# Kernel tuning notes

Hardware: AMD Instinct MI355X
Metric: run time of the kernel (lower is better)

## Reference

```python
import jax, jax.numpy as jnp
import numpy as np

N, FIN, H, C, D = 50000, 128, 4, 64, 4
E = 800000


def leaky_relu(x, slope):
    return jnp.where(x >= 0, x, slope * x)


def gat_layer(x, src, dst, W, A, att_src, att_dst, bias):
    # x: [N, Fin]; W: [Fin, H*C]; A: [Fin, H*D]; att_*: [H, D]; bias: [C]
    n = x.shape[0]
    h = (x @ W).reshape(n, H, -1)          # [N, H, C] message features
    a = (x @ A).reshape(n, H, -1)          # [N, H, D] attention features
    alpha_src = jnp.einsum('nhd,hd->nh', a, att_src)   # [N, H]
    alpha_dst = jnp.einsum('nhd,hd->nh', a, att_dst)   # [N, H]
    e = leaky_relu(alpha_src[src] + alpha_dst[dst], 0.2)  # [E, H]
    # edge softmax over incoming edges of each destination node
    m = jax.ops.segment_max(e, dst, num_segments=n)       # [N, H]
    ex = jnp.exp(e - m[dst])                               # [E, H]
    denom = jax.ops.segment_sum(ex, dst, num_segments=n)  # [N, H]
    w = ex / denom[dst]                                    # [E, H]
    msg = h[src] * w[..., None]                            # [E, H, C]
    out = jax.ops.segment_sum(msg, dst, num_segments=n)   # [N, H, C]
    return out.mean(axis=1) + bias                         # head-average -> [N, C]


def setup_inputs() -> dict:
    key = jax.random.key(0)
    ks = jax.random.split(key, 12)
    x = jax.random.normal(ks[0], (N, FIN), dtype=jnp.float32)
    edge_index = jax.random.randint(ks[1], (2, E), 0, N, dtype=jnp.int64)
    s = 0.05
    return {
        'x': x,
        'edge_index': edge_index,
        'W1': jax.random.normal(ks[2], (FIN, H * C), dtype=jnp.float32) * s,
        'A1': jax.random.normal(ks[3], (FIN, H * D), dtype=jnp.float32) * s,
        'att_src1': jax.random.normal(ks[4], (H, D), dtype=jnp.float32) * s,
        'att_dst1': jax.random.normal(ks[5], (H, D), dtype=jnp.float32) * s,
        'b1': jnp.zeros((C,), dtype=jnp.float32),
        'W2': jax.random.normal(ks[6], (C, H * C), dtype=jnp.float32) * s,
        'A2': jax.random.normal(ks[7], (C, H * D), dtype=jnp.float32) * s,
        'att_src2': jax.random.normal(ks[8], (H, D), dtype=jnp.float32) * s,
        'att_dst2': jax.random.normal(ks[9], (H, D), dtype=jnp.float32) * s,
        'b2': jnp.zeros((C,), dtype=jnp.float32),
    }


def reference(x, edge_index, W1, A1, att_src1, att_dst1, b1, W2, A2, att_src2, att_dst2, b2):
    src, dst = edge_index[0], edge_index[1]
    x = gat_layer(x, src, dst, W1, A1, att_src1, att_dst1, b1)
    x = leaky_relu(x, 0.1)
    x = gat_layer(x, src, dst, W2, A2, att_src2, att_dst2, b2)
    x = leaky_relu(x, 0.1)
    return x
```

## Files before the change

kernel.cpp:

```cpp
#include <hip/hip_runtime.h>


#define N_NODES 50000
#define N_EDGES 800000
#define CAP 64
#define NB_SC4 782
#define NB_NODE1 782

typedef __attribute__((ext_vector_type(8))) short short8;
typedef __attribute__((ext_vector_type(8))) _Float16 f16x8;
typedef __attribute__((ext_vector_type(2))) _Float16 f16x2;
typedef __attribute__((ext_vector_type(4))) float f32x4;
typedef __attribute__((ext_vector_type(8))) unsigned short ushort8;
typedef __attribute__((ext_vector_type(4))) unsigned short us4v;

__device__ __forceinline__ float bf2f(unsigned short u){
  return __uint_as_float(((unsigned int)u) << 16);
}
__device__ __forceinline__ unsigned short f2bf(float f){
  unsigned int u = __float_as_uint(f);
  u = (u + 0x7FFFu + ((u >> 16) & 1u)) >> 16;
  return (unsigned short)u;
}
__device__ __forceinline__ float ldf(const void* p, int i, bool bf){
  return bf ? bf2f(((const unsigned short*)p)[i]) : ((const float*)p)[i];
}
__device__ __forceinline__ float rdlane(float v, int lane){
  return __uint_as_float(__builtin_amdgcn_readlane(__float_as_uint(v), lane));
}

struct SetupPtrs {
  const void *W1, *A1, *aS1, *aD1, *b1, *W2, *A2, *aS2, *aD2, *b2, *x;
};

__global__ __launch_bounds__(256) void k_setup(SetupPtrs S,
    _Float16* __restrict__ Wb1f, _Float16* __restrict__ Wb2f,
    unsigned short* __restrict__ Bsd1f, unsigned short* __restrict__ Bsd2f,
    float* __restrict__ bc1, float* __restrict__ bc2,
    int* __restrict__ flag)
{
  __shared__ int sbf;
  const int tid = threadIdx.x;
  if (tid < 64){
    unsigned int w = ((const unsigned int*)S.x)[tid] & 0xFFFFu;
    unsigned int e = (w >> 7) & 0xFFu;
    bool hit = (e >= 100u && e <= 135u);
    unsigned long long m = __ballot(hit);
    if (tid == 0) sbf = (__popcll(m) > 40) ? 1 : 0;
  }
  __syncthreads();
  const bool bf = (sbf != 0);
  const int bw = blockIdx.x;
  if (bw < 128){
    int t = bw * 256 + tid;
    int j = t & 7, lane = (t >> 3) & 63, kt = (t >> 9) & 15, nt = t >> 13;
    int q = kt * 32 + (lane >> 4) * 8 + j;
    int c = nt * 16 + (lane & 15);
    int h = q >> 7, f = q & 127;
    Wb1f[t] = (_Float16)(0.25f * ldf(S.W1, f * 256 + h * 64 + c, bf));
  } else if (bw < 192){
    int t = (bw - 128) * 256 + tid;
    int j = t & 7, lane = (t >> 3) & 63, kt = (t >> 9) & 7, nt = t >> 12;
    int q = kt * 32 + (lane >> 4) * 8 + j;
    int c = nt * 16 + (lane & 15);
    int h = q >> 6, f = q & 63;
    Wb2f[t] = (_Float16)(0.25f * ldf(S.W2, f * 256 + h * 64 + c, bf));
  } else if (bw < 200){
    int t = (bw - 192) * 256 + tid;
    int j = t & 7, lane = (t >> 3) & 63, kt = t >> 9;
    int k = kt * 32 + (lane >> 4) * 8 + j;
    int c = lane & 15;
    float v = 0.f;
    if (c < 4){
      for (int dd = 0; dd < 4; ++dd)
        v += ldf(S.A1, k * 16 + c * 4 + dd, bf) * ldf(S.aS1, c * 4 + dd, bf);
    } else if (c < 8){
      int h = c - 4;
      for (int dd = 0; dd < 4; ++dd)
        v += ldf(S.A1, k * 16 + h * 4 + dd, bf) * ldf(S.aD1, h * 4 + dd, bf);
    }
    Bsd1f[t] = f2bf(v);
  } else if (bw < 204){
    int t = (bw - 200) * 256 + tid;
    int j = t & 7, lane = (t >> 3) & 63, kt = t >> 9;
    int k = kt * 32 + (lane >> 4) * 8 + j;
    int c = lane & 15;
    float v = 0.f;
    if (c < 4){
      for (int dd = 0; dd < 4; ++dd)
        v += ldf(S.A2, k * 16 + c * 4 + dd, bf) * ldf(S.aS2, c * 4 + dd, bf);
    } else if (c < 8){
      int h = c - 4;
      for (int dd = 0; dd < 4; ++dd)
        v += ldf(S.A2, k * 16 + h * 4 + dd, bf) * ldf(S.aD2, h * 4 + dd, bf);
    }
    Bsd2f[t] = f2bf(v);
  } else {
    if (tid < 64)       bc1[tid] = ldf(S.b1, tid, bf);
    else if (tid < 128) bc2[tid - 64] = ldf(S.b2, tid - 64, bf);
    else if (tid == 128) *flag = bf ? 1 : 0;
  }
}


template<int F, bool DYN>
__device__ __forceinline__ void nodeA_body(int nblk, int tid,
    const void* __restrict__ xin_, const unsigned short* __restrict__ Bsdf,
    float* __restrict__ alpha_s, float* __restrict__ alpha_d,
    const int* __restrict__ flag)
{
  const int STR = F + 8;
  const int KT  = F / 32;
  const int CH  = F / 8;
  __shared__ unsigned short xs[64 * (F + 8)];
  const int base = nblk * 64;
  bool bf = true;
  if (DYN) bf = (*flag != 0);
  for (int v = tid; v < 64 * CH; v += 256){
    int row = v / CH, c8 = v % CH;
    int node = base + row; if (node >= N_NODES) node = N_NODES - 1;
    size_t g = (size_t)node * F + c8 * 8;
    ushort8 u;
    if (!DYN || bf){
      u = *(const ushort8*)((const unsigned short*)xin_ + g);
    } else {
      const float* xf = (const float*)xin_ + g;
      float4 f0 = *(const float4*)xf, f1 = *(const float4*)(xf + 4);
      u[0]=f2bf(f0.x); u[1]=f2bf(f0.y); u[2]=f2bf(f0.z); u[3]=f2bf(f0.w);
      u[4]=f2bf(f1.x); u[5]=f2bf(f1.y); u[6]=f2bf(f1.z); u[7]=f2bf(f1.w);
    }
    *(ushort8*)&xs[row * STR + c8 * 8] = u;
  }
  __syncthreads();

  const int wave = tid >> 6, l = tid & 63;
  const int quad = l >> 4, m = l & 15;
  const int wbase = base + wave * 16;

  f32x4 aacc = (f32x4)0.f;
  #pragma unroll
  for (int kt = 0; kt < KT; ++kt){
    short8 af = *(const short8*)&xs[(wave * 16 + m) * STR + kt * 32 + quad * 8];
    short8 sdfrag = *(const short8*)(Bsdf + ((size_t)kt * 64 + l) * 8);
    aacc = __builtin_amdgcn_mfma_f32_16x16x32_bf16(af, sdfrag, aacc, 0, 0, 0);
  }
  if (m < 8){
    float* dstp = (m < 4) ? alpha_s : alpha_d;
    int hh = m & 3;
    #pragma unroll
    for (int r = 0; r < 4; ++r){
      int node = wbase + quad * 4 + r;
      if (node < N_NODES) dstp[node * 4 + hh] = aacc[r];
    }
  }
}


__global__ __launch_bounds__(256) void k_scatter_nodeA1(
    const int* __restrict__ src, const int* __restrict__ dst,
    int* __restrict__ fill, unsigned short* __restrict__ csr,
    const void* __restrict__ xin_, const unsigned short* __restrict__ Bsdf,
    float* __restrict__ alpha_s, float* __restrict__ alpha_d,
    const int* __restrict__ flag)
{
  const int b = blockIdx.x, tid = threadIdx.x;
  if (b < NB_SC4){
    const int ebase = b * 1024 + tid;
    int d[4], s[4];
    #pragma unroll
    for (int i = 0; i < 4; ++i){
      int e = ebase + i * 256;
      bool ok = (e < N_EDGES);
      d[i] = ok ? dst[e] : -1;
      s[i] = ok ? src[e] : 0;
    }
    #pragma unroll
    for (int i = 0; i < 4; ++i){
      if (d[i] >= 0){
        int r = atomicAdd(&fill[d[i]], 1);
        if (r < CAP) csr[((unsigned)d[i] << 6) + r] = (unsigned short)s[i];
      }
    }
    return;
  }
  nodeA_body<128, true>(b - NB_SC4, tid, xin_, Bsdf, alpha_s, alpha_d, flag);
}

template<int F, bool DYN>
__global__ __launch_bounds__(256) void k_nodeA(const void* __restrict__ xin_,
    const unsigned short* __restrict__ Bsdf,
    float* __restrict__ alpha_s, float* __restrict__ alpha_d,
    const int* __restrict__ flag)
{
  nodeA_body<F, DYN>(blockIdx.x, threadIdx.x, xin_, Bsdf, alpha_s, alpha_d, flag);
}


template<int FIN, bool BF>
__device__ __forceinline__ void ldrow(const void* xg, unsigned s, int f0,
                                      float (&out)[FIN / 16])
{
  const int NFL = FIN / 16;
  if (BF){
    const unsigned short* p = (const unsigned short*)xg + (size_t)s * FIN + f0;
    if (NFL == 8){
      ushort8 u = *(const ushort8*)p;
      #pragma unroll
      for (int j = 0; j < NFL; ++j) out[j] = bf2f(u[j]);
    } else {
      us4v u = *(const us4v*)p;
      #pragma unroll
      for (int j = 0; j < NFL; ++j) out[j] = bf2f(u[j]);
    }
  } else {
    const float* p = (const float*)xg + (size_t)s * FIN + f0;
    #pragma unroll
    for (int j = 0; j < NFL; ++j) out[j] = p[j];
  }
}

template<bool BF, int STR>
__device__ __forceinline__ void aggr_phase1_u128(const void* __restrict__ xg,
    const float* __restrict__ alpha_s, const float* __restrict__ alpha_d,
    const int* __restrict__ fill, const unsigned short* __restrict__ csr,
    _Float16* __restrict__ ylds, int base, int w, int l)
{
  const int h = l >> 4;
  #pragma unroll 1
  for (int r = 0; r < 4; ++r){
    const int n = base + w * 4 + r;
    const float adv = alpha_d[n * 4 + h];
    float den = 0.f;
    float acc[4][2];
    #pragma unroll
    for (int hh = 0; hh < 4; ++hh){ acc[hh][0] = 0.f; acc[hh][1] = 0.f; }

    int cnt = fill[n]; if (cnt > CAP) cnt = CAP;
    const unsigned short* cp = csr + ((unsigned)n << 6);
    int p = 0;
    for (; p + 8 <= cnt; p += 8){
      ushort8 s8 = *(const ushort8*)(cp + p);
      float a[8];
      float lo[8], hi[8];
      #pragma unroll
      for (int i = 0; i < 8; ++i){
        unsigned s = s8[i];
        a[i] = alpha_s[s * 4 + h];
        if (BF){
          unsigned xv = *(const unsigned int*)((const unsigned short*)xg + (size_t)s * 128 + 2 * l);
          lo[i] = bf2f((unsigned short)(xv & 0xFFFFu));
          hi[i] = bf2f((unsigned short)(xv >> 16));
        } else {
          const float* xf = (const float*)xg + (size_t)s * 128 + 2 * l;
          lo[i] = xf[0]; hi[i] = xf[1];
        }
      }
      #pragma unroll
      for (int i = 0; i < 8; ++i){
        float e = a[i] + adv; e = fmaxf(e, 0.2f * e); float wt = __expf(e);
        den += wt;
        float w0 = rdlane(wt, 0),  w1 = rdlane(wt, 16);
        float w2 = rdlane(wt, 32), w3 = rdlane(wt, 48);
        acc[0][0] += w0 * lo[i]; acc[0][1] += w0 * hi[i];
        acc[1][0] += w1 * lo[i]; acc[1][1] += w1 * hi[i];
        acc[2][0] += w2 * lo[i]; acc[2][1] += w2 * hi[i];
        acc[3][0] += w3 * lo[i]; acc[3][1] += w3 * hi[i];
      }
    }
    if (p + 4 <= cnt){
      ushort4 s4 = *(const ushort4*)(cp + p);
      unsigned ss[4] = {s4.x, s4.y, s4.z, s4.w};
      float a[4], lo[4], hi[4];
      #pragma unroll
      for (int i = 0; i < 4; ++i){
        a[i] = alpha_s[ss[i] * 4 + h];
        if (BF){
          unsigned xv = *(const unsigned int*)((const unsigned short*)xg + (size_t)ss[i] * 128 + 2 * l);
          lo[i] = bf2f((unsigned short)(xv & 0xFFFFu));
          hi[i] = bf2f((unsigned short)(xv >> 16));
        } else {
          const float* xf = (const float*)xg + (size_t)ss[i] * 128 + 2 * l;
          lo[i] = xf[0]; hi[i] = xf[1];
        }
      }
      #pragma unroll
      for (int i = 0; i < 4; ++i){
        float e = a[i] + adv; e = fmaxf(e, 0.2f * e); float wt = __expf(e);
        den += wt;
        float w0 = rdlane(wt, 0),  w1 = rdlane(wt, 16);
        float w2 = rdlane(wt, 32), w3 = rdlane(wt, 48);
        acc[0][0] += w0 * lo[i]; acc[0][1] += w0 * hi[i];
        acc[1][0] += w1 * lo[i]; acc[1][1] += w1 * hi[i];
        acc[2][0] += w2 * lo[i]; acc[2][1] += w2 * hi[i];
        acc[3][0] += w3 * lo[i]; acc[3][1] += w3 * hi[i];
      }
      p += 4;
    }
    for (; p < cnt; ++p){
      unsigned s = cp[p];
      float a = alpha_s[s * 4 + h];
      float lo, hi;
      if (BF){
        unsigned xv = *(const unsigned int*)((const unsigned short*)xg + (size_t)s * 128 + 2 * l);
        lo = bf2f((unsigned short)(xv & 0xFFFFu));
        hi = bf2f((unsigned short)(xv >> 16));
      } else {
        const float* xf = (const float*)xg + (size_t)s * 128 + 2 * l;
        lo = xf[0]; hi = xf[1];
      }
      float e = a + adv; e = fmaxf(e, 0.2f * e); float wt = __expf(e);
      den += wt;
      float w0 = rdlane(wt, 0),  w1 = rdlane(wt, 16);
      float w2 = rdlane(wt, 32), w3 = rdlane(wt, 48);
      acc[0][0] += w0 * lo; acc[0][1] += w0 * hi;
      acc[1][0] += w1 * lo; acc[1][1] += w1 * hi;
      acc[2][0] += w2 * lo; acc[2][1] += w2 * hi;
      acc[3][0] += w3 * lo; acc[3][1] += w3 * hi;
    }
    float d0 = rdlane(den, 0),  d1 = rdlane(den, 16);
    float d2 = rdlane(den, 32), d3 = rdlane(den, 48);
    float rh0 = (d0 > 0.f) ? (1.f / d0) : 0.f;
    float rh1 = (d1 > 0.f) ? (1.f / d1) : 0.f;
    float rh2 = (d2 > 0.f) ? (1.f / d2) : 0.f;
    float rh3 = (d3 > 0.f) ? (1.f / d3) : 0.f;
    const int row = w * 4 + r;
    _Float16* yp = &ylds[row * STR + 2 * l];
    *(f16x2*)(yp +   0) = (f16x2){(_Float16)(acc[0][0] * rh0), (_Float16)(acc[0][1] * rh0)};
    *(f16x2*)(yp + 128) = (f16x2){(_Float16)(acc[1][0] * rh1), (_Float16)(acc[1][1] * rh1)};
    *(f16x2*)(yp + 256) = (f16x2){(_Float16)(acc[2][0] * rh2), (_Float16)(acc[2][1] * rh2)};
    *(f16x2*)(yp + 384) = (f16x2){(_Float16)(acc[3][0] * rh3), (_Float16)(acc[3][1] * rh3)};
  }
}

template<int FIN, bool BF, int STR>
__device__ __forceinline__ void aggr_phase1(const void* __restrict__ xg,
    const float* __restrict__ alpha_s, const float* __restrict__ alpha_d,
    const int* __restrict__ fill, const unsigned short* __restrict__ csr,
    _Float16* __restrict__ ylds, int base, int w, int l)
{
  const int NFL = FIN / 16;
  const int h = l >> 4, sub = l & 15, f0 = sub * NFL;
  #pragma unroll 1
  for (int r = 0; r < 4; ++r){
    const int n = base + w * 4 + r;
    const float adv = alpha_d[n * 4 + h];
    float den = 0.f;
    float acc[NFL];
    #pragma unroll
    for (int j = 0; j < NFL; ++j) acc[j] = 0.f;

    int cnt = fill[n]; if (cnt > CAP) cnt = CAP;
    const unsigned short* cp = csr + ((unsigned)n << 6);
    int p = 0;
    for (; p + 8 <= cnt; p += 8){
      ushort8 s8 = *(const ushort8*)(cp + p);
      float a[8];
      float v[8][NFL];
      #pragma unroll
      for (int i = 0; i < 8; ++i){
        unsigned s = s8[i];
        a[i] = alpha_s[s * 4 + h];
        ldrow<FIN, BF>(xg, s, f0, v[i]);
      }
      #pragma unroll
      for (int i = 0; i < 8; ++i){
        float e = a[i] + adv; e = fmaxf(e, 0.2f * e); float wt = __expf(e);
        den += wt;
        #pragma unroll
        for (int j = 0; j < NFL; ++j) acc[j] += wt * v[i][j];
      }
    }
    if (p + 4 <= cnt){
      ushort4 s4 = *(const ushort4*)(cp + p);
      unsigned sx = s4.x, sy = s4.y, sz = s4.z, sw = s4.w;
      float ax = alpha_s[sx * 4 + h];
      float ay = alpha_s[sy * 4 + h];
      float az = alpha_s[sz * 4 + h];
      float aw = alpha_s[sw * 4 + h];
      float vx[NFL], vy[NFL], vz[NFL], vw[NFL];
      ldrow<FIN, BF>(xg, sx, f0, vx);
      ldrow<FIN, BF>(xg, sy, f0, vy);
      ldrow<FIN, BF>(xg, sz, f0, vz);
      ldrow<FIN, BF>(xg, sw, f0, vw);
      float e0 = ax + adv; e0 = fmaxf(e0, 0.2f * e0); float w0 = __expf(e0);
      float e1 = ay + adv; e1 = fmaxf(e1, 0.2f * e1); float w1 = __expf(e1);
      float e2 = az + adv; e2 = fmaxf(e2, 0.2f * e2); float w2 = __expf(e2);
      float e3 = aw + adv; e3 = fmaxf(e3, 0.2f * e3); float w3 = __expf(e3);
      den += w0; den += w1; den += w2; den += w3;
      #pragma unroll
      for (int j = 0; j < NFL; ++j)
        acc[j] += w0 * vx[j] + w1 * vy[j] + w2 * vz[j] + w3 * vw[j];
      p += 4;
    }
    for (; p < cnt; ++p){
      unsigned s = cp[p];
      float a = alpha_s[s * 4 + h];
      float v0[NFL];
      ldrow<FIN, BF>(xg, s, f0, v0);
      float e = a + adv; e = fmaxf(e, 0.2f * e); float wgt = __expf(e);
      den += wgt;
      #pragma unroll
      for (int j = 0; j < NFL; ++j) acc[j] += wgt * v0[j];
    }
    const float rh = (den > 0.f) ? (1.f / den) : 0.f;
    const int row = w * 4 + r;
    _Float16* yp = &ylds[row * STR + h * FIN + f0];
    #pragma unroll
    for (int j = 0; j < NFL; ++j) yp[j] = (_Float16)(acc[j] * rh);
  }
}

template<int FIN, int MODE>
__global__ __launch_bounds__(256) void k_aggrX(
    const void* __restrict__ xg,
    const float* __restrict__ alpha_s, const float* __restrict__ alpha_d,
    const int* __restrict__ fill, const unsigned short* __restrict__ csr,
    const _Float16* __restrict__ Wf,
    const float* __restrict__ bias, void* __restrict__ out,
    const int* __restrict__ flag)
{
  const int K = 4 * FIN, KT = K / 32, STR = K + 8;
  __shared__ _Float16 ylds[16 * (4 * FIN + 8)];
  const int tid = threadIdx.x, w = tid >> 6, l = tid & 63;
  const int base = blockIdx.x * 16;

  if (FIN == 128){
    if (MODE == 0 && *flag == 0)
      aggr_phase1_u128<false, STR>(xg, alpha_s, alpha_d, fill, csr, ylds, base, w, l);
    else
      aggr_phase1_u128<true,  STR>(xg, alpha_s, alpha_d, fill, csr, ylds, base, w, l);
  } else {
    if (MODE == 0 && *flag == 0)
      aggr_phase1<FIN, false, STR>(xg, alpha_s, alpha_d, fill, csr, ylds, base, w, l);
    else
      aggr_phase1<FIN, true,  STR>(xg, alpha_s, alpha_d, fill, csr, ylds, base, w, l);
  }
  __syncthreads();

  const int quad = l >> 4, m = l & 15;
  const int nt = w;
  f32x4 cacc = (f32x4)0.f;
  #pragma unroll
  for (int kt = 0; kt < KT; ++kt){
    f16x8 av = *(const f16x8*)&ylds[m * STR + kt * 32 + quad * 8];
    f16x8 bv = *(const f16x8*)(Wf + ((size_t)(nt * KT + kt) * 64 + l) * 8);
    cacc = __builtin_amdgcn_mfma_f32_16x16x32_f16(av, bv, cacc, 0, 0, 0);
  }
  const int c = nt * 16 + m;
  const float bs = bias[c];
  #pragma unroll
  for (int r2 = 0; r2 < 4; ++r2){
    int node = base + quad * 4 + r2;
    float v = cacc[r2] + bs;
    v = fmaxf(v, 0.1f * v);
    if (MODE == 0){
      ((unsigned short*)out)[(size_t)node * 64 + c] = f2bf(v);
    } else {
      if (*flag) ((unsigned short*)out)[(size_t)node * 64 + c] = f2bf(v);
      else       ((float*)out)[(size_t)node * 64 + c] = v;
    }
  }
}


extern "C" void kernel_launch(void* const* d_in, const int* in_sizes, int n_in,
                              void* d_out, int out_size, void* d_ws, size_t ws_size,
                              hipStream_t stream)
{
  const void* x  = d_in[0];
  const int* ei  = (const int*)d_in[1];
  const int* src = ei;
  const int* dst = ei + N_EDGES;

  char* ws = (char*)d_ws;
  unsigned short* csr = (unsigned short*)(ws);
  unsigned short* x2  = (unsigned short*)(ws + 6400000);
  float* as_    = (float*)(ws + 12800000);
  float* ad_    = (float*)(ws + 13600000);
  int*   fill   = (int*)  (ws + 14400000);
  _Float16* Wb1f = (_Float16*)(ws + 14600000);
  _Float16* Wb2f = (_Float16*)(ws + 14665536);
  unsigned short* Bsd1f = (unsigned short*)(ws + 14698304);
  unsigned short* Bsd2f = (unsigned short*)(ws + 14702400);
  float* bc1    = (float*)(ws + 14704448);
  float* bc2    = (float*)(ws + 14704704);
  int*   flag   = (int*)  (ws + 14704960);

  hipMemsetAsync(fill, 0, N_NODES * sizeof(int), stream);

  SetupPtrs S;
  S.W1 = d_in[2];  S.A1 = d_in[3];  S.aS1 = d_in[4];  S.aD1 = d_in[5];  S.b1 = d_in[6];
  S.W2 = d_in[7];  S.A2 = d_in[8];  S.aS2 = d_in[9];  S.aD2 = d_in[10]; S.b2 = d_in[11];
  S.x  = x;
  k_setup<<<205, 256, 0, stream>>>(S, Wb1f, Wb2f, Bsd1f, Bsd2f, bc1, bc2, flag);

  k_scatter_nodeA1<<<NB_SC4 + NB_NODE1, 256, 0, stream>>>(
      src, dst, fill, csr, x, Bsd1f, as_, ad_, flag);

  k_aggrX<128, 0><<<N_NODES / 16, 256, 0, stream>>>(
      x, as_, ad_, fill, csr, Wb1f, bc1, x2, flag);

  k_nodeA<64, false><<<NB_NODE1, 256, 0, stream>>>(x2, Bsd2f, as_, ad_, flag);

  k_aggrX<64, 1><<<N_NODES / 16, 256, 0, stream>>>(
      x2, as_, ad_, fill, csr, Wb2f, bc2, d_out, flag);
}
```

Before: 284.1 us.

## Fuse layer-2 attention projection into layer-1 aggregation epilogue; specialise 64-wide gather

Layer 2's attention-logit computation (the k_nodeA launch) is folded into the epilogue of layer-1's aggregation kernel. The just-computed bf16 output tile is staged in LDS and one wave runs an MFMA against the layer-2 src/dst attention projection, writing alpha into separate buffers. This removes a kernel launch and a re-read of x2. The layer-2 gather is also rewritten so each lane loads one feature of each neighbour and gets per-head weights by lane broadcast, replacing the generic 4-element-per-lane path. The cost is extra LDS, a second block barrier and more work in layer-1's tail.

```diff
diff --git a/kernel.cpp b/kernel.cpp
--- a/kernel.cpp
+++ b/kernel.cpp
@@ -103,25 +103,21 @@
 }
 
 
-template<int F, bool DYN>
 __device__ __forceinline__ void nodeA_body(int nblk, int tid,
     const void* __restrict__ xin_, const unsigned short* __restrict__ Bsdf,
     float* __restrict__ alpha_s, float* __restrict__ alpha_d,
     const int* __restrict__ flag)
 {
-  const int STR = F + 8;
-  const int KT  = F / 32;
-  const int CH  = F / 8;
-  __shared__ unsigned short xs[64 * (F + 8)];
+  const int F = 128, STR = F + 8, KT = 4, CH = F / 8;
+  __shared__ unsigned short xs[64 * 136];
   const int base = nblk * 64;
-  bool bf = true;
-  if (DYN) bf = (*flag != 0);
+  const bool bf = (*flag != 0);
   for (int v = tid; v < 64 * CH; v += 256){
     int row = v / CH, c8 = v % CH;
     int node = base + row; if (node >= N_NODES) node = N_NODES - 1;
     size_t g = (size_t)node * F + c8 * 8;
     ushort8 u;
-    if (!DYN || bf){
+    if (bf){
       u = *(const ushort8*)((const unsigned short*)xin_ + g);
     } else {
       const float* xf = (const float*)xin_ + g;
@@ -183,41 +179,9 @@
     }
     return;
   }
-  nodeA_body<128, true>(b - NB_SC4, tid, xin_, Bsdf, alpha_s, alpha_d, flag);
-}
-
-template<int F, bool DYN>
-__global__ __launch_bounds__(256) void k_nodeA(const void* __restrict__ xin_,
-    const unsigned short* __restrict__ Bsdf,
-    float* __restrict__ alpha_s, float* __restrict__ alpha_d,
-    const int* __restrict__ flag)
-{
-  nodeA_body<F, DYN>(blockIdx.x, threadIdx.x, xin_, Bsdf, alpha_s, alpha_d, flag);
-}
-
-
-template<int FIN, bool BF>
-__device__ __forceinline__ void ldrow(const void* xg, unsigned s, int f0,
-                                      float (&out)[FIN / 16])
-{
-  const int NFL = FIN / 16;
-  if (BF){
-    const unsigned short* p = (const unsigned short*)xg + (size_t)s * FIN + f0;
-    if (NFL == 8){
-      ushort8 u = *(const ushort8*)p;
-      #pragma unroll
-      for (int j = 0; j < NFL; ++j) out[j] = bf2f(u[j]);
-    } else {
-      us4v u = *(const us4v*)p;
-      #pragma unroll
-      for (int j = 0; j < NFL; ++j) out[j] = bf2f(u[j]);
-    }
-  } else {
-    const float* p = (const float*)xg + (size_t)s * FIN + f0;
-    #pragma unroll
-    for (int j = 0; j < NFL; ++j) out[j] = p[j];
-  }
-}
+  nodeA_body(b - NB_SC4, tid, xin_, Bsdf, alpha_s, alpha_d, flag);
+}
+
 
 template<bool BF, int STR>
 __device__ __forceinline__ void aggr_phase1_u128(const void* __restrict__ xg,
@@ -332,81 +296,85 @@
   }
 }
 
-template<int FIN, bool BF, int STR>
-__device__ __forceinline__ void aggr_phase1(const void* __restrict__ xg,
+template<int STR>
+__device__ __forceinline__ void aggr_phase1_u64(const unsigned short* __restrict__ xg,
     const float* __restrict__ alpha_s, const float* __restrict__ alpha_d,
     const int* __restrict__ fill, const unsigned short* __restrict__ csr,
     _Float16* __restrict__ ylds, int base, int w, int l)
 {
-  const int NFL = FIN / 16;
-  const int h = l >> 4, sub = l & 15, f0 = sub * NFL;
+  const int h = l >> 4;
   #pragma unroll 1
   for (int r = 0; r < 4; ++r){
     const int n = base + w * 4 + r;
     const float adv = alpha_d[n * 4 + h];
     float den = 0.f;
-    float acc[NFL];
-    #pragma unroll
-    for (int j = 0; j < NFL; ++j) acc[j] = 0.f;
+    float acc[4] = {0.f, 0.f, 0.f, 0.f};
 
     int cnt = fill[n]; if (cnt > CAP) cnt = CAP;
     const unsigned short* cp = csr + ((unsigned)n << 6);
     int p = 0;
     for (; p + 8 <= cnt; p += 8){
       ushort8 s8 = *(const ushort8*)(cp + p);
-      float a[8];
-      float v[8][NFL];
+      float a[8], xv[8];
       #pragma unroll
       for (int i = 0; i < 8; ++i){
         unsigned s = s8[i];
         a[i] = alpha_s[s * 4 + h];
-        ldrow<FIN, BF>(xg, s, f0, v[i]);
+        xv[i] = bf2f(xg[(size_t)s * 64 + l]);
       }
       #pragma unroll
       for (int i = 0; i < 8; ++i){
         float e = a[i] + adv; e = fmaxf(e, 0.2f * e); float wt = __expf(e);
         den += wt;
-        #pragma unroll
-        for (int j = 0; j < NFL; ++j) acc[j] += wt * v[i][j];
+        float w0 = rdlane(wt, 0),  w1 = rdlane(wt, 16);
+        float w2 = rdlane(wt, 32), w3 = rdlane(wt, 48);
+        acc[0] += w0 * xv[i]; acc[1] += w1 * xv[i];
+        acc[2] += w2 * xv[i]; acc[3] += w3 * xv[i];
       }
     }
     if (p + 4 <= cnt){
       ushort4 s4 = *(const ushort4*)(cp + p);
-      unsigned sx = s4.x, sy = s4.y, sz = s4.z, sw = s4.w;
-      float ax = alpha_s[sx * 4 + h];
-      float ay = alpha_s[sy * 4 + h];
-      float az = alpha_s[sz * 4 + h];
-      float aw = alpha_s[sw * 4 + h];
-      float vx[NFL], vy[NFL], vz[NFL], vw[NFL];
-      ldrow<FIN, BF>(xg, sx, f0, vx);
-      ldrow<FIN, BF>(xg, sy, f0, vy);
-      ldrow<FIN, BF>(xg, sz, f0, vz);
-      ldrow<FIN, BF>(xg, sw, f0, vw);
-      float e0 = ax + adv; e0 = fmaxf(e0, 0.2f * e0); float w0 = __expf(e0);
-      float e1 = ay + adv; e1 = fmaxf(e1, 0.2f * e1); float w1 = __expf(e1);
-      float e2 = az + adv; e2 = fmaxf(e2, 0.2f * e2); float w2 = __expf(e2);
-      float e3 = aw + adv; e3 = fmaxf(e3, 0.2f * e3); float w3 = __expf(e3);
-      den += w0; den += w1; den += w2; den += w3;
-      #pragma unroll
-      for (int j = 0; j < NFL; ++j)
-        acc[j] += w0 * vx[j] + w1 * vy[j] + w2 * vz[j] + w3 * vw[j];
+      unsigned ss[4] = {s4.x, s4.y, s4.z, s4.w};
+      float a[4], xv[4];
+      #pragma unroll
+      for (int i = 0; i < 4; ++i){
+        a[i] = alpha_s[ss[i] * 4 + h];
+        xv[i] = bf2f(xg[(size_t)ss[i] * 64 + l]);
+      }
+      #pragma unroll
+      for (int i = 0; i < 4; ++i){
+        float e = a[i] + adv; e = fmaxf(e, 0.2f * e); float wt = __expf(e);
+        den += wt;
+        float w0 = rdlane(wt, 0),  w1 = rdlane(wt, 16);
+        float w2 = rdlane(wt, 32), w3 = rdlane(wt, 48);
+        acc[0] += w0 * xv[i]; acc[1] += w1 * xv[i];
+        acc[2] += w2 * xv[i]; acc[3] += w3 * xv[i];
+      }
       p += 4;
     }
     for (; p < cnt; ++p){
       unsigned s = cp[p];
       float a = alpha_s[s * 4 + h];
-      float v0[NFL];
-      ldrow<FIN, BF>(xg, s, f0, v0);
-      float e = a + adv; e = fmaxf(e, 0.2f * e); float wgt = __expf(e);
-      den += wgt;
-      #pragma unroll
-      for (int j = 0; j < NFL; ++j) acc[j] += wgt * v0[j];
-    }
-    const float rh = (den > 0.f) ? (1.f / den) : 0.f;
+      float xv = bf2f(xg[(size_t)s * 64 + l]);
+      float e = a + adv; e = fmaxf(e, 0.2f * e); float wt = __expf(e);
+      den += wt;
+      float w0 = rdlane(wt, 0),  w1 = rdlane(wt, 16);
+      float w2 = rdlane(wt, 32), w3 = rdlane(wt, 48);
+      acc[0] += w0 * xv; acc[1] += w1 * xv;
+      acc[2] += w2 * xv; acc[3] += w3 * xv;
+    }
+    float d0 = rdlane(den, 0),  d1 = rdlane(den, 16);
+    float d2 = rdlane(den, 32), d3 = rdlane(den, 48);
+    float rh0 = (d0 > 0.f) ? (1.f / d0) : 0.f;
+    float rh1 = (d1 > 0.f) ? (1.f / d1) : 0.f;
+    float rh2 = (d2 > 0.f) ? (1.f / d2) : 0.f;
+    float rh3 = (d3 > 0.f) ? (1.f / d3) : 0.f;
     const int row = w * 4 + r;
-    _Float16* yp = &ylds[row * STR + h * FIN + f0];
-    #pragma unroll
-    for (int j = 0; j < NFL; ++j) yp[j] = (_Float16)(acc[j] * rh);
+    _Float16* yp = &ylds[row * STR + l];
+    yp[0]   = (_Float16)(acc[0] * rh0);
+    yp[64]  = (_Float16)(acc[1] * rh1);
+    yp[128] = (_Float16)(acc[2] * rh2);
+    yp[192] = (_Float16)(acc[3] * rh3);
   }
 }
 
@@ -417,10 +385,13 @@
     const int* __restrict__ fill, const unsigned short* __restrict__ csr,
     const _Float16* __restrict__ Wf,
     const float* __restrict__ bias, void* __restrict__ out,
-    const int* __restrict__ flag)
+    const int* __restrict__ flag,
+    const unsigned short* __restrict__ Bsd2f,
+    float* __restrict__ as2, float* __restrict__ ad2)
 {
   const int K = 4 * FIN, KT = K / 32, STR = K + 8;
   __shared__ _Float16 ylds[16 * (4 * FIN + 8)];
+  __shared__ unsigned short x2t[16 * 72];
   const int tid = threadIdx.x, w = tid >> 6, l = tid & 63;
   const int base = blockIdx.x * 16;
 
@@ -430,10 +401,7 @@
     else
       aggr_phase1_u128<true,  STR>(xg, alpha_s, alpha_d, fill, csr, ylds, base, w, l);
   } else {
-    if (MODE == 0 && *flag == 0)
-      aggr_phase1<FIN, false, STR>(xg, alpha_s, alpha_d, fill, csr, ylds, base, w, l);
-    else
-      aggr_phase1<FIN, true,  STR>(xg, alpha_s, alpha_d, fill, csr, ylds, base, w, l);
+    aggr_phase1_u64<STR>((const unsigned short*)xg, alpha_s, alpha_d, fill, csr, ylds, base, w, l);
   }
   __syncthreads();
 
@@ -454,10 +422,34 @@
     float v = cacc[r2] + bs;
     v = fmaxf(v, 0.1f * v);
     if (MODE == 0){
-      ((unsigned short*)out)[(size_t)node * 64 + c] = f2bf(v);
+      unsigned short o = f2bf(v);
+      ((unsigned short*)out)[(size_t)node * 64 + c] = o;
+      x2t[(quad * 4 + r2) * 72 + c] = o;
     } else {
       if (*flag) ((unsigned short*)out)[(size_t)node * 64 + c] = f2bf(v);
       else       ((float*)out)[(size_t)node * 64 + c] = v;
+    }
+  }
+
+  if (MODE == 0){
+    __syncthreads();
+    if (w == 0){
+      f32x4 aacc = (f32x4)0.f;
+      #pragma unroll
+      for (int kt = 0; kt < 2; ++kt){
+        short8 af = *(const short8*)&x2t[m * 72 + kt * 32 + quad * 8];
+        short8 sd = *(const short8*)(Bsd2f + ((size_t)kt * 64 + l) * 8);
+        aacc = __builtin_amdgcn_mfma_f32_16x16x32_bf16(af, sd, aacc, 0, 0, 0);
+      }
+      if (m < 8){
+        float* dstp = (m < 4) ? as2 : ad2;
+        int hh = m & 3;
+        #pragma unroll
+        for (int r = 0; r < 4; ++r){
+          int node = base + quad * 4 + r;
+          dstp[node * 4 + hh] = aacc[r];
+        }
+      }
     }
   }
 }
@@ -477,14 +469,16 @@
   unsigned short* x2  = (unsigned short*)(ws + 6400000);
   float* as_    = (float*)(ws + 12800000);
   float* ad_    = (float*)(ws + 13600000);
-  int*   fill   = (int*)  (ws + 14400000);
-  _Float16* Wb1f = (_Float16*)(ws + 14600000);
-  _Float16* Wb2f = (_Float16*)(ws + 14665536);
-  unsigned short* Bsd1f = (unsigned short*)(ws + 14698304);
-  unsigned short* Bsd2f = (unsigned short*)(ws + 14702400);
-  float* bc1    = (float*)(ws + 14704448);
-  float* bc2    = (float*)(ws + 14704704);
-  int*   flag   = (int*)  (ws + 14704960);
+  float* as2_   = (float*)(ws + 14400000);
+  float* ad2_   = (float*)(ws + 15200000);
+  int*   fill   = (int*)  (ws + 16000000);
+  _Float16* Wb1f = (_Float16*)(ws + 16200000);
+  _Float16* Wb2f = (_Float16*)(ws + 16265536);
+  unsigned short* Bsd1f = (unsigned short*)(ws + 16298304);
+  unsigned short* Bsd2f = (unsigned short*)(ws + 16302400);
+  float* bc1    = (float*)(ws + 16304448);
+  float* bc2    = (float*)(ws + 16304704);
+  int*   flag   = (int*)  (ws + 16304960);
 
   hipMemsetAsync(fill, 0, N_NODES * sizeof(int), stream);
 
@@ -498,10 +492,8 @@
       src, dst, fill, csr, x, Bsd1f, as_, ad_, flag);
 
   k_aggrX<128, 0><<<N_NODES / 16, 256, 0, stream>>>(
-      x, as_, ad_, fill, csr, Wb1f, bc1, x2, flag);
-
-  k_nodeA<64, false><<<NB_NODE1, 256, 0, stream>>>(x2, Bsd2f, as_, ad_, flag);
+      x, as_, ad_, fill, csr, Wb1f, bc1, x2, flag, Bsd2f, as2_, ad2_);
 
   k_aggrX<64, 1><<<N_NODES / 16, 256, 0, stream>>>(
-      x2, as_, ad_, fill, csr, Wb2f, bc2, d_out, flag);
-}
+      x2, as2_, ad2_, fill, csr, Wb2f, bc2, d_out, flag, Bsd2f, as2_, ad2_);
+}
```

Result: faster. 277.1 us (-2.5%).
